# Optimization experiments

Hardware: AMD Instinct MI355X
Metric: run time of the kernel (lower is better)

The kernel has to match this reference:

```python
import jax, jax.numpy as jnp
import numpy as np

LEAK = 0.2
NUM_GRAPHS = 64


def _gat(h_in, src, dst, eh, W, att_src, att_dst, att_edge, lin_edge_W, bias, N):
    # PyG GATConv with edge_dim, concat=False (mean over heads)
    H, C = att_src.shape
    h = (h_in @ W).reshape(N, H, C)                      # [N,H,C]
    e = (eh @ lin_edge_W).reshape(-1, H, C)              # [Eaug,H,C]
    a_s = jnp.einsum('nhc,hc->nh', h, att_src)           # [N,H]
    a_d = jnp.einsum('nhc,hc->nh', h, att_dst)
    a_e = jnp.einsum('ehc,hc->eh', e, att_edge)          # [Eaug,H]
    score = jax.nn.leaky_relu(a_s[src] + a_d[dst] + a_e, LEAK)
    # scatter-softmax over incoming edges of each destination node
    m = jax.ops.segment_max(score, dst, num_segments=N)
    ex = jnp.exp(score - m[dst])
    den = jax.ops.segment_sum(ex, dst, num_segments=N)
    alpha = ex / den[dst]                                # [Eaug,H]
    out = jax.ops.segment_sum(alpha[:, :, None] * h[src], dst, num_segments=N)
    return out.mean(axis=1) + bias                       # concat=False -> head mean


def setup_inputs() -> dict:
    key = jax.random.key(0)
    ks = jax.random.split(key, 32)
    N, E, F, FE, HID, H, NT = 30000, 480000, 64, 16, 64, 4, 16
    Cin1 = F + HID
    s = 0.05
    d = {
        'x': jax.random.normal(ks[0], (N, F), jnp.float32),
        'edge_attr': jax.random.normal(ks[1], (E, FE), jnp.float32),
        'node_emb': jax.random.normal(ks[2], (NT, HID), jnp.float32) * s,
        'edge_W': jax.random.normal(ks[3], (FE, HID), jnp.float32) * s,
        'edge_b': jnp.zeros((HID,), jnp.float32),
        'W1': jax.random.normal(ks[4], (Cin1, H * HID), jnp.float32) * s,
        'as1': jax.random.normal(ks[5], (H, HID), jnp.float32) * s,
        'ad1': jax.random.normal(ks[6], (H, HID), jnp.float32) * s,
        'ae1': jax.random.normal(ks[7], (H, HID), jnp.float32) * s,
        'leW1': jax.random.normal(ks[8], (HID, H * HID), jnp.float32) * s,
        'b1': jnp.zeros((HID,), jnp.float32),
        'W2': jax.random.normal(ks[9], (HID, H * HID), jnp.float32) * s,
        'as2': jax.random.normal(ks[10], (H, HID), jnp.float32) * s,
        'ad2': jax.random.normal(ks[11], (H, HID), jnp.float32) * s,
        'ae2': jax.random.normal(ks[12], (H, HID), jnp.float32) * s,
        'leW2': jax.random.normal(ks[13], (HID, H * HID), jnp.float32) * s,
        'b2': jnp.zeros((HID,), jnp.float32),
        'sage_Wl': jax.random.normal(ks[14], (HID, HID), jnp.float32) * s,
        'sage_bl': jnp.zeros((HID,), jnp.float32),
        'sage_Wr': jax.random.normal(ks[15], (HID, HID), jnp.float32) * s,
        'lin1_W': jax.random.normal(ks[16], (HID, HID), jnp.float32) * s,
        'lin1_b': jnp.zeros((HID,), jnp.float32),
        'lin2_W': jax.random.normal(ks[17], (HID, HID), jnp.float32) * s,
        'lin2_b': jnp.zeros((HID,), jnp.float32),
        'tel_W': jax.random.normal(ks[18], (HID, 1), jnp.float32) * s,
        'tel_b': jnp.zeros((1,), jnp.float32),
        'comp_W': jax.random.normal(ks[19], (HID, 1), jnp.float32) * s,
        'comp_b': jnp.zeros((1,), jnp.float32),
        'pch_W': jax.random.normal(ks[20], (HID, 1), jnp.float32) * s,
        'pch_b': jnp.zeros((1,), jnp.float32),
        'edge_index': jax.random.randint(ks[21], (2, E), 0, N, jnp.int32),
        'batch': jnp.sort(jax.random.randint(ks[22], (N,), 0, NUM_GRAPHS, jnp.int32)),
        'node_type': jax.random.randint(ks[23], (N,), 0, NT, jnp.int32),
    }
    return d


def reference(x, edge_attr, node_emb, edge_W, edge_b,
              W1, as1, ad1, ae1, leW1, b1,
              W2, as2, ad2, ae2, leW2, b2,
              sage_Wl, sage_bl, sage_Wr,
              lin1_W, lin1_b, lin2_W, lin2_b,
              tel_W, tel_b, comp_W, comp_b, pch_W, pch_b,
              edge_index, batch, node_type):
    N = x.shape[0]
    src0, dst0 = edge_index[0], edge_index[1]

    h0 = jnp.concatenate([x, node_emb[node_type]], axis=-1)   # [N, F+HID]
    eh = edge_attr @ edge_W + edge_b                          # [E, HID]

    # GATConv default add_self_loops=True, fill_value='mean' on edge_attr
    loop = jnp.arange(N, dtype=src0.dtype)
    src = jnp.concatenate([src0, loop])
    dst = jnp.concatenate([dst0, loop])
    eh_aug = jnp.concatenate([eh, jnp.broadcast_to(eh.mean(axis=0), (N, eh.shape[1]))], axis=0)

    h1 = jax.nn.elu(_gat(h0, src, dst, eh_aug, W1, as1, ad1, ae1, leW1, b1, N))
    h2 = jax.nn.elu(_gat(h1, src, dst, eh_aug, W2, as2, ad2, ae2, leW2, b2, N))

    # SAGEConv: mean neighbor aggregation (src->dst) + root transform
    deg = jax.ops.segment_sum(jnp.ones_like(dst0, dtype=h2.dtype), dst0, num_segments=N)
    agg = jax.ops.segment_sum(h2[src0], dst0, num_segments=N) / jnp.clip(deg, 1.0)[:, None]
    h3 = jax.nn.elu(agg @ sage_Wl + sage_bl + h2 @ sage_Wr)

    # global mean pool per graph
    cnt = jax.ops.segment_sum(jnp.ones((N,), h3.dtype), batch, num_segments=NUM_GRAPHS)
    g = jax.ops.segment_sum(h3, batch, num_segments=NUM_GRAPHS) / jnp.clip(cnt, 1.0)[:, None]

    g = jax.nn.elu(g @ lin1_W + lin1_b)                       # dropout inactive (eval)
    g = g @ lin2_W + lin2_b
    return (g @ tel_W + tel_b, g @ comp_W + comp_b, g @ pch_W + pch_b)
```

## Files before the change

### kernel.cpp

```cpp
#include <hip/hip_runtime.h>
#include <math.h>

#define NN 30000
#define NE 480000
#define FEA 16
#define HID 64
#define NG 64
#define LEAKK 0.2f

#define S_MEANEA 0
#define S_KF1    16
#define S_C1     80
#define S_AEL1   84
#define S_KF2    88
#define S_C2     152
#define S_AEL2   156
#define S_MS1    160
#define S_MD1    672
#define S_MS2    1184
#define S_MD2    1440

__device__ __forceinline__ float eluf(float v) { return v > 0.f ? v : expm1f(v); }
__device__ __forceinline__ float leakyf(float v) { return v >= 0.f ? v : LEAKK * v; }
__device__ __forceinline__ void fma4(float4& a, float w, const float4& x) {
    a.x += w * x.x; a.y += w * x.y; a.z += w * x.z; a.w += w * x.w;
}
__device__ __forceinline__ unsigned bf16pack(float a, float b) {
    unsigned ua = __float_as_uint(a), ub = __float_as_uint(b);
    ua = (ua + 0x7FFFu + ((ua >> 16) & 1u)) >> 16;
    ub = (ub + 0x7FFFu + ((ub >> 16) & 1u)) >> 16;
    return ua | (ub << 16);
}
__device__ __forceinline__ float4 bf16x4(uint2 p) {
    float4 r;
    r.x = __uint_as_float(p.x << 16);
    r.y = __uint_as_float(p.x & 0xFFFF0000u);
    r.z = __uint_as_float(p.y << 16);
    r.w = __uint_as_float(p.y & 0xFFFF0000u);
    return r;
}

__global__ __launch_bounds__(256) void cm_prepw_kernel(
    const int* __restrict__ dst, const float* __restrict__ EA,
    int* __restrict__ cnt, int* __restrict__ rank, float* __restrict__ S,
    const float* __restrict__ W1, const float* __restrict__ W2,
    const float* __restrict__ Wl, const float* __restrict__ Wr,
    const float* __restrict__ emb,
    float* __restrict__ WC1, float* __restrict__ WC2, float* __restrict__ B128) {
    __shared__ float red[1024];
    int t = threadIdx.x;
    if (blockIdx.x < 176) {
        int i = blockIdx.x * 256 + t;
        if (i < 16384) {
            int hk = i >> 6, c = i & 63;
            int h = hk >> 6, k = hk & 63;
            WC1[i] = 0.25f * W1[k * 256 + h * 64 + c];
        } else if (i < 20480) {
            int j2 = i - 16384;
            int r2 = j2 >> 6, c = j2 & 63;
            int h = r2 >> 4, tau = r2 & 15;
            float v = 0.f;
            for (int j = 0; j < 64; j++)
                v += emb[tau * 64 + j] * W1[(64 + j) * 256 + h * 64 + c];
            WC1[i] = 0.25f * v;
        } else if (i < 36864) {
            int j = i - 20480;
            int hk = j >> 6, c = j & 63;
            int h = hk >> 6, k = hk & 63;
            WC2[j] = 0.25f * W2[k * 256 + h * 64 + c];
        } else if (i < 45056) {
            int j = i - 36864;
            int k = j >> 6, c = j & 63;
            B128[j] = (k < 64) ? Wl[k * 64 + c] : Wr[(k - 64) * 64 + c];
        }
        return;
    }
    int base = (blockIdx.x - 176) * 512;
#pragma unroll
    for (int i = 0; i < 2; i++) {
        int e = base + i * 256 + t;
        if (e < NE) rank[e] = atomicAdd(&cnt[dst[e]], 1);
    }
    int c4 = t & 3;
    int rbase = base + (t >> 2);
    float4 acc = {0, 0, 0, 0};
#pragma unroll
    for (int i = 0; i < 8; i++) {
        int r = rbase + i * 64;
        if (r < NE) {
            float4 v = *(const float4*)(EA + (size_t)r * FEA + c4 * 4);
            acc.x += v.x; acc.y += v.y; acc.z += v.z; acc.w += v.w;
        }
    }
    *(float4*)&red[t * 4] = acc;
    __syncthreads();
    if (t < 16) {
        int grp = t >> 2;
        int comp = t & 3;
        float sum = 0.f;
        for (int j = 0; j < 64; j++) sum += red[(grp + 4 * j) * 4 + comp];
        atomicAdd(&S[S_MEANEA + grp * 4 + comp], sum);
    }
}

__global__ void scan_blocks_kernel(const int* __restrict__ cnt, int* __restrict__ eoff,
                                   int* __restrict__ bsum) {
    __shared__ int wsum[16];
    int t = threadIdx.x;
    int i = blockIdx.x * 1024 + t;
    int v = (i < NN) ? cnt[i] : 0;
    int lane = t & 63;
    int incl = v;
#pragma unroll
    for (int ofs = 1; ofs < 64; ofs <<= 1) {
        int u = __shfl_up(incl, ofs, 64);
        if (lane >= ofs) incl += u;
    }
    int wid = t >> 6;
    if (lane == 63) wsum[wid] = incl;
    __syncthreads();
    if (t < 16) {
        int s = wsum[t];
#pragma unroll
        for (int ofs = 1; ofs < 16; ofs <<= 1) {
            int u = __shfl_up(s, ofs, 64);
            if (t >= ofs) s += u;
        }
        wsum[t] = s;
    }
    __syncthreads();
    int excl = incl - v + (wid > 0 ? wsum[wid - 1] : 0);
    if (i < NN) eoff[i] = excl;
    if (t == 1023) bsum[blockIdx.x] = excl + v;
}

__global__ void tops_goff_prep_kernel(
    const int* __restrict__ bsum, int* __restrict__ boff, int nb,
    const int* __restrict__ batch, int* __restrict__ goff,
    const float* __restrict__ W1, const float* __restrict__ as1, const float* __restrict__ ad1,
    const float* __restrict__ ae1, const float* __restrict__ leW1,
    const float* __restrict__ W2, const float* __restrict__ as2, const float* __restrict__ ad2,
    const float* __restrict__ ae2, const float* __restrict__ leW2,
    const float* __restrict__ edge_W, const float* __restrict__ edge_b,
    float* __restrict__ S) {
    __shared__ float M1[256], M2[256], meh[64];
    int t = threadIdx.x;
    if (blockIdx.x == 0) {
        if (t >= 64) return;
        int v = (t < nb) ? bsum[t] : 0;
        int incl = v;
#pragma unroll
        for (int ofs = 1; ofs < 64; ofs <<= 1) {
            int u = __shfl_up(incl, ofs, 64);
            if (t >= ofs) incl += u;
        }
        boff[t] = incl - v;
        return;
    }
    if (blockIdx.x == 1) {
        if (t > NG) return;
        int lo = 0, hi = NN;
        while (lo < hi) {
            int mid = (lo + hi) >> 1;
            if (batch[mid] < t) lo = mid + 1; else hi = mid;
        }
        goff[t] = lo;
        return;
    }
    if (t < 16) S[S_MEANEA + t] *= (1.0f / (float)NE);
    __syncthreads();
    {
        int k = t >> 2, h = t & 3;
        float m1 = 0.f, m2 = 0.f;
        for (int c = 0; c < 64; c++) {
            m1 += leW1[k * 256 + h * 64 + c] * ae1[h * 64 + c];
            m2 += leW2[k * 256 + h * 64 + c] * ae2[h * 64 + c];
        }
        M1[t] = m1; M2[t] = m2;
    }
    if (t < 64) {
        float v = edge_b[t];
        for (int f = 0; f < FEA; f++) v += S[S_MEANEA + f] * edge_W[f * 64 + t];
        meh[t] = v;
    }
    __syncthreads();
    if (t < 64) {
        int f = t >> 2, h = t & 3;
        float k1 = 0.f, k2 = 0.f;
        for (int k = 0; k < 64; k++) {
            k1 += edge_W[f * 64 + k] * M1[k * 4 + h];
            k2 += edge_W[f * 64 + k] * M2[k * 4 + h];
        }
        S[S_KF1 + t] = k1; S[S_KF2 + t] = k2;
    } else if (t < 68) {
        int h = t - 64;
        float c1 = 0.f, c2 = 0.f, a1 = 0.f, a2 = 0.f;
        for (int k = 0; k < 64; k++) {
            c1 += edge_b[k] * M1[k * 4 + h];
            c2 += edge_b[k] * M2[k * 4 + h];
            a1 += meh[k] * M1[k * 4 + h];
            a2 += meh[k] * M2[k * 4 + h];
        }
        S[S_C1 + h] = c1; S[S_C2 + h] = c2;
        S[S_AEL1 + h] = a1; S[S_AEL2 + h] = a2;
    }
    for (int i = t; i < 512; i += 256) {
        int k = i >> 2, h = i & 3;
        float s = 0.f, d = 0.f;
        for (int c = 0; c < 64; c++) {
            float w = W1[k * 256 + h * 64 + c];
            s += w * as1[h * 64 + c];
            d += w * ad1[h * 64 + c];
        }
        S[S_MS1 + i] = s; S[S_MD1 + i] = d;
    }
    for (int i = t; i < 256; i += 256) {
        int k = i >> 2, h = i & 3;
        float s = 0.f, d = 0.f;
        for (int c = 0; c < 64; c++) {
            float w = W2[k * 256 + h * 64 + c];
            s += w * as2[h * 64 + c];
            d += w * ad2[h * 64 + c];
        }
        S[S_MS2 + i] = s; S[S_MD2 + i] = d;
    }
}

__global__ __launch_bounds__(256) void scanadd_attn_kernel(
    const int* __restrict__ boff, int* __restrict__ eoff,
    const float* __restrict__ x, const float* __restrict__ node_emb,
    const int* __restrict__ node_type, const float* __restrict__ S,
    float* __restrict__ as_, float* __restrict__ ad_, unsigned* __restrict__ xb) {
    __shared__ float xt[64 * 132];
    __shared__ float ms[512], md[512];
    __shared__ int ntS[64];
    int t = threadIdx.x;
    if (blockIdx.x < 118) {
        int i = blockIdx.x * 256 + t;
        if (i < NN) eoff[i] += boff[i >> 10];
        if (i == 0) eoff[NN] = NE;
        return;
    }
    int n0 = (blockIdx.x - 118) * 64;
    if (t < 64) {
        int n = n0 + t;
        ntS[t] = (n < NN) ? node_type[n] : 0;
    }
    for (int i = t; i < 512; i += 256) { ms[i] = S[S_MS1 + i]; md[i] = S[S_MD1 + i]; }
    __syncthreads();
    for (int i = t; i < 1024; i += 256) {
        int r = i >> 4, c4 = (i & 15) * 4;
        int n = n0 + r;
        float4 f = {0, 0, 0, 0};
        if (n < NN) f = *(const float4*)(x + (size_t)n * 64 + c4);
        *(float4*)&xt[r * 132 + c4] = f;
    }
    for (int i = t; i < 1024; i += 256) {
        int r = i >> 4, c4 = (i & 15) * 4;
        int n = n0 + r;
        float4 f = {0, 0, 0, 0};
        if (n < NN) f = *(const float4*)(node_emb + (size_t)ntS[r] * 64 + c4);
        *(float4*)&xt[r * 132 + 64 + c4] = f;
    }
    __syncthreads();
    for (int i = t; i < 2048; i += 256) {
        int r = i >> 5, u = i & 31;
        int n = n0 + r;
        if (n < NN)
            xb[(size_t)n * 32 + u] = bf16pack(xt[r * 132 + 2 * u], xt[r * 132 + 2 * u + 1]);
    }
    int r = t >> 2, h = t & 3;
    float s = 0.f, d = 0.f;
#pragma unroll 8
    for (int k = 0; k < 128; k++) {
        float xv = xt[r * 132 + k];
        s += xv * ms[k * 4 + h];
        d += xv * md[k * 4 + h];
    }
    int n = n0 + r;
    if (n < NN) { as_[n * 4 + h] = s; ad_[n * 4 + h] = d; }
}

__global__ void scatter_score_kernel(const int* __restrict__ src, const int* __restrict__ dst,
                                     const float* __restrict__ EA, const float* __restrict__ S,
                                     const float* __restrict__ as_, const float* __restrict__ ad_,
                                     const int* __restrict__ node_type,
                                     const int* __restrict__ eoff, const int* __restrict__ rank,
                                     int2* __restrict__ se_sorted,
                                     float* __restrict__ sc1, float* __restrict__ ae2s) {
    int e = blockIdx.x * 256 + threadIdx.x;
    if (e >= NE) return;
    int s = src[e], d = dst[e];
    float a1[4], a2[4];
#pragma unroll
    for (int h = 0; h < 4; h++) { a1[h] = S[S_C1 + h]; a2[h] = S[S_C2 + h]; }
    const float4* EA4 = (const float4*)(EA + (size_t)e * FEA);
#pragma unroll
    for (int q = 0; q < 4; q++) {
        float4 v = EA4[q];
        float vv[4] = {v.x, v.y, v.z, v.w};
#pragma unroll
        for (int j = 0; j < 4; j++) {
            int f = q * 4 + j;
#pragma unroll
            for (int h = 0; h < 4; h++) {
                a1[h] += vv[j] * S[S_KF1 + f * 4 + h];
                a2[h] += vv[j] * S[S_KF2 + f * 4 + h];
            }
        }
    }
    ((float4*)ae2s)[e] = make_float4(a2[0], a2[1], a2[2], a2[3]);
    float4 asv = ((const float4*)as_)[s];
    float4 adv = ((const float4*)ad_)[d];
    float4 r;
    r.x = expf(leakyf(asv.x + adv.x + a1[0]));
    r.y = expf(leakyf(asv.y + adv.y + a1[1]));
    r.z = expf(leakyf(asv.z + adv.z + a1[2]));
    r.w = expf(leakyf(asv.w + adv.w + a1[3]));
    ((float4*)sc1)[e] = r;
    int ty = node_type[s];
    se_sorted[eoff[d] + rank[e]] = make_int2(s, e | (ty << 24));
}

__global__ void score2_kernel(const int* __restrict__ src, const int* __restrict__ dst,
                              const float* __restrict__ ae2s,
                              const float* __restrict__ as_, const float* __restrict__ ad_,
                              float* __restrict__ sc2) {
    int e = blockIdx.x * 256 + threadIdx.x;
    if (e >= NE) return;
    int s = src[e], d = dst[e];
    float4 ae = ((const float4*)ae2s)[e];
    float4 asv = ((const float4*)as_)[s];
    float4 adv = ((const float4*)ad_)[d];
    float4 r;
    r.x = expf(leakyf(asv.x + adv.x + ae.x));
    r.y = expf(leakyf(asv.y + adv.y + ae.y));
    r.z = expf(leakyf(asv.z + adv.z + ae.z));
    r.w = expf(leakyf(asv.w + adv.w + ae.w));
    ((float4*)sc2)[e] = r;
}

__global__ __launch_bounds__(256) void agg_gat1_kernel(
    const int* __restrict__ eoff, const int2* __restrict__ se_sorted,
    const float* __restrict__ sc1, const unsigned* __restrict__ xb,
    const int* __restrict__ node_type,
    const float* __restrict__ as_, const float* __restrict__ ad_,
    const float* __restrict__ Sael, float* __restrict__ agg) {
    int n = blockIdx.x * 4 + (threadIdx.x >> 6);
    if (n >= NN) return;
    int lane = threadIdx.x & 63;
    int sub = lane >> 4, ch = lane & 15;
    const uint2* Xb = (const uint2*)xb;
    const float4* W4 = (const float4*)sc1;
    float4 asn = ((const float4*)as_)[n];
    float4 adn = ((const float4*)ad_)[n];
    float4 a0 = {0, 0, 0, 0}, a1 = a0, a2 = a0, a3 = a0, dn = a0, tw = a0;
    int b = eoff[n], e_end = eoff[n + 1];
    int nE = e_end - b;
    int i = sub;
    for (; i + 4 < nE; i += 8) {
        int2 se0 = se_sorted[b + i], se1 = se_sorted[b + i + 4];
        int e0 = se0.y & 0xFFFFFF, t0 = se0.y >> 24;
        int e1 = se1.y & 0xFFFFFF, t1 = se1.y >> 24;
        float4 w0 = W4[e0], w1 = W4[e1];
        float4 x0 = bf16x4(Xb[(size_t)se0.x * 16 + ch]);
        float4 x1 = bf16x4(Xb[(size_t)se1.x * 16 + ch]);
        fma4(a0, w0.x, x0); fma4(a1, w0.y, x0); fma4(a2, w0.z, x0); fma4(a3, w0.w, x0);
        fma4(a0, w1.x, x1); fma4(a1, w1.y, x1); fma4(a2, w1.z, x1); fma4(a3, w1.w, x1);
        dn.x += w0.x + w1.x; dn.y += w0.y + w1.y;
        dn.z += w0.z + w1.z; dn.w += w0.w + w1.w;
        if (ch == t0) { tw.x += w0.x; tw.y += w0.y; tw.z += w0.z; tw.w += w0.w; }
        if (ch == t1) { tw.x += w1.x; tw.y += w1.y; tw.z += w1.z; tw.w += w1.w; }
    }
    for (; i < nE; i += 4) {
        int2 se0 = se_sorted[b + i];
        int e0 = se0.y & 0xFFFFFF, t0 = se0.y >> 24;
        float4 w0 = W4[e0];
        float4 x0 = bf16x4(Xb[(size_t)se0.x * 16 + ch]);
        fma4(a0, w0.x, x0); fma4(a1, w0.y, x0); fma4(a2, w0.z, x0); fma4(a3, w0.w, x0);
        dn.x += w0.x; dn.y += w0.y; dn.z += w0.z; dn.w += w0.w;
        if (ch == t0) { tw.x += w0.x; tw.y += w0.y; tw.z += w0.z; tw.w += w0.w; }
    }
    if (sub == 0) {
        float e0 = expf(leakyf(asn.x + adn.x + Sael[0]));
        float e1 = expf(leakyf(asn.y + adn.y + Sael[1]));
        float e2 = expf(leakyf(asn.z + adn.z + Sael[2]));
        float e3 = expf(leakyf(asn.w + adn.w + Sael[3]));
        float4 xs = bf16x4(Xb[(size_t)n * 16 + ch]);
        fma4(a0, e0, xs); fma4(a1, e1, xs); fma4(a2, e2, xs); fma4(a3, e3, xs);
        dn.x += e0; dn.y += e1; dn.z += e2; dn.w += e3;
        int tn = node_type[n];
        if (ch == tn) { tw.x += e0; tw.y += e1; tw.z += e2; tw.w += e3; }
    }
#pragma unroll
    for (int mask = 16; mask < 64; mask <<= 1) {
        a0.x += __shfl_xor(a0.x, mask, 64); a0.y += __shfl_xor(a0.y, mask, 64);
        a0.z += __shfl_xor(a0.z, mask, 64); a0.w += __shfl_xor(a0.w, mask, 64);
        a1.x += __shfl_xor(a1.x, mask, 64); a1.y += __shfl_xor(a1.y, mask, 64);
        a1.z += __shfl_xor(a1.z, mask, 64); a1.w += __shfl_xor(a1.w, mask, 64);
        a2.x += __shfl_xor(a2.x, mask, 64); a2.y += __shfl_xor(a2.y, mask, 64);
        a2.z += __shfl_xor(a2.z, mask, 64); a2.w += __shfl_xor(a2.w, mask, 64);
        a3.x += __shfl_xor(a3.x, mask, 64); a3.y += __shfl_xor(a3.y, mask, 64);
        a3.z += __shfl_xor(a3.z, mask, 64); a3.w += __shfl_xor(a3.w, mask, 64);
        dn.x += __shfl_xor(dn.x, mask, 64); dn.y += __shfl_xor(dn.y, mask, 64);
        dn.z += __shfl_xor(dn.z, mask, 64); dn.w += __shfl_xor(dn.w, mask, 64);
        tw.x += __shfl_xor(tw.x, mask, 64); tw.y += __shfl_xor(tw.y, mask, 64);
        tw.z += __shfl_xor(tw.z, mask, 64); tw.w += __shfl_xor(tw.w, mask, 64);
    }
    if (sub == 0) {
        float i0 = 1.f / dn.x, i1 = 1.f / dn.y, i2 = 1.f / dn.z, i3 = 1.f / dn.w;
        float* A = agg + (size_t)n * 320;
        float4* A4 = (float4*)A;
        A4[ch]      = make_float4(a0.x * i0, a0.y * i0, a0.z * i0, a0.w * i0);
        A4[16 + ch] = make_float4(a1.x * i1, a1.y * i1, a1.z * i1, a1.w * i1);
        A4[32 + ch] = make_float4(a2.x * i2, a2.y * i2, a2.z * i2, a2.w * i2);
        A4[48 + ch] = make_float4(a3.x * i3, a3.y * i3, a3.z * i3, a3.w * i3);
        A[256 + ch]      = tw.x * i0;
        A[256 + 16 + ch] = tw.y * i1;
        A[256 + 32 + ch] = tw.z * i2;
        A[256 + 48 + ch] = tw.w * i3;
    }
}

__global__ __launch_bounds__(256) void agg_gat2_kernel(
    const int* __restrict__ eoff, const int2* __restrict__ se_sorted,
    const float* __restrict__ sc2, const unsigned* __restrict__ h1b,
    const float* __restrict__ as_, const float* __restrict__ ad_,
    const float* __restrict__ Sael, float* __restrict__ agg) {
    int n = blockIdx.x * 4 + (threadIdx.x >> 6);
    if (n >= NN) return;
    int lane = threadIdx.x & 63;
    int sub = lane >> 4, ch = lane & 15;
    const uint2* Xb = (const uint2*)h1b;
    const float4* W4 = (const float4*)sc2;
    float4 asn = ((const float4*)as_)[n];
    float4 adn = ((const float4*)ad_)[n];
    float4 a0 = {0, 0, 0, 0}, a1 = a0, a2 = a0, a3 = a0, dn = a0;
    int b = eoff[n], e = eoff[n + 1];
    int nE = e - b;
    int i = sub;
    for (; i + 4 < nE; i += 8) {
        int2 se0 = se_sorted[b + i], se1 = se_sorted[b + i + 4];
        float4 w0 = W4[se0.y & 0xFFFFFF], w1 = W4[se1.y & 0xFFFFFF];
        float4 x0 = bf16x4(Xb[(size_t)se0.x * 16 + ch]);
        float4 x1 = bf16x4(Xb[(size_t)se1.x * 16 + ch]);
        fma4(a0, w0.x, x0); fma4(a1, w0.y, x0); fma4(a2, w0.z, x0); fma4(a3, w0.w, x0);
        fma4(a0, w1.x, x1); fma4(a1, w1.y, x1); fma4(a2, w1.z, x1); fma4(a3, w1.w, x1);
        dn.x += w0.x + w1.x; dn.y += w0.y + w1.y;
        dn.z += w0.z + w1.z; dn.w += w0.w + w1.w;
    }
    for (; i < nE; i += 4) {
        int2 se0 = se_sorted[b + i];
        float4 w0 = W4[se0.y & 0xFFFFFF];
        float4 x0 = bf16x4(Xb[(size_t)se0.x * 16 + ch]);
        fma4(a0, w0.x, x0); fma4(a1, w0.y, x0); fma4(a2, w0.z, x0); fma4(a3, w0.w, x0);
        dn.x += w0.x; dn.y += w0.y; dn.z += w0.z; dn.w += w0.w;
    }
    if (sub == 0) {
        float e0 = expf(leakyf(asn.x + adn.x + Sael[0]));
        float e1 = expf(leakyf(asn.y + adn.y + Sael[1]));
        float e2 = expf(leakyf(asn.z + adn.z + Sael[2]));
        float e3 = expf(leakyf(asn.w + adn.w + Sael[3]));
        float4 xs = bf16x4(Xb[(size_t)n * 16 + ch]);
        fma4(a0, e0, xs); fma4(a1, e1, xs); fma4(a2, e2, xs); fma4(a3, e3, xs);
        dn.x += e0; dn.y += e1; dn.z += e2; dn.w += e3;
    }
#pragma unroll
    for (int mask = 16; mask < 64; mask <<= 1) {
        a0.x += __shfl_xor(a0.x, mask, 64); a0.y += __shfl_xor(a0.y, mask, 64);
        a0.z += __shfl_xor(a0.z, mask, 64); a0.w += __shfl_xor(a0.w, mask, 64);
        a1.x += __shfl_xor(a1.x, mask, 64); a1.y += __shfl_xor(a1.y, mask, 64);
        a1.z += __shfl_xor(a1.z, mask, 64); a1.w += __shfl_xor(a1.w, mask, 64);
        a2.x += __shfl_xor(a2.x, mask, 64); a2.y += __shfl_xor(a2.y, mask, 64);
        a2.z += __shfl_xor(a2.z, mask, 64); a2.w += __shfl_xor(a2.w, mask, 64);
        a3.x += __shfl_xor(a3.x, mask, 64); a3.y += __shfl_xor(a3.y, mask, 64);
        a3.z += __shfl_xor(a3.z, mask, 64); a3.w += __shfl_xor(a3.w, mask, 64);
        dn.x += __shfl_xor(dn.x, mask, 64); dn.y += __shfl_xor(dn.y, mask, 64);
        dn.z += __shfl_xor(dn.z, mask, 64); dn.w += __shfl_xor(dn.w, mask, 64);
    }
    if (sub == 0) {
        float i0 = 1.f / dn.x, i1 = 1.f / dn.y, i2 = 1.f / dn.z, i3 = 1.f / dn.w;
        float4* agg4 = (float4*)(agg + (size_t)n * 256);
        agg4[ch]      = make_float4(a0.x * i0, a0.y * i0, a0.z * i0, a0.w * i0);
        agg4[16 + ch] = make_float4(a1.x * i1, a1.y * i1, a1.z * i1, a1.w * i1);
        agg4[32 + ch] = make_float4(a2.x * i2, a2.y * i2, a2.z * i2, a2.w * i2);
        agg4[48 + ch] = make_float4(a3.x * i3, a3.y * i3, a3.z * i3, a3.w * i3);
    }
}

template <int K, bool DOATT>
__global__ __launch_bounds__(256) void gemm64_kernel(
    const float* __restrict__ A, const float* __restrict__ B,
    const float* __restrict__ bias, float* __restrict__ out,
    unsigned* __restrict__ out16,
    const float* __restrict__ ms_g, const float* __restrict__ md_g,
    float* __restrict__ as_, float* __restrict__ ad_) {
    __shared__ float As[2][32 * 68];
    __shared__ float Bs[2][32 * 68];
    __shared__ float msS[256], mdS[256];
    int t = threadIdx.x;
    int tx = t & 15, ty = t >> 4;
    int m_base = blockIdx.x * 64;
    if (DOATT) { msS[t] = ms_g[t]; mdS[t] = md_g[t]; }
    int arow0 = t >> 3, akq0 = (t & 7) * 4;
    int arow1 = (t + 256) >> 3, akq1 = ((t + 256) & 7) * 4;
    int bkr = t >> 4, bnc = (t & 15) * 4;
    int am0 = m_base + arow0, am1 = m_base + arow1;
    float4 fa0, fa1, fb0, fb1;
    fa0 = (am0 < NN) ? *(const float4*)(A + (size_t)am0 * K + akq0) : make_float4(0, 0, 0, 0);
    fa1 = (am1 < NN) ? *(const float4*)(A + (size_t)am1 * K + akq1) : make_float4(0, 0, 0, 0);
    fb0 = *(const float4*)(B + (size_t)bkr * 64 + bnc);
    fb1 = *(const float4*)(B + (size_t)(bkr + 16) * 64 + bnc);
    As[0][(akq0 + 0) * 68 + arow0] = fa0.x;
    As[0][(akq0 + 1) * 68 + arow0] = fa0.y;
    As[0][(akq0 + 2) * 68 + arow0] = fa0.z;
    As[0][(akq0 + 3) * 68 + arow0] = fa0.w;
    As[0][(akq1 + 0) * 68 + arow1] = fa1.x;
    As[0][(akq1 + 1) * 68 + arow1] = fa1.y;
    As[0][(akq1 + 2) * 68 + arow1] = fa1.z;
    As[0][(akq1 + 3) * 68 + arow1] = fa1.w;
    *(float4*)&Bs[0][bkr * 68 + bnc] = fb0;
    *(float4*)&Bs[0][(bkr + 16) * 68 + bnc] = fb1;
    __syncthreads();
    float acc[4][4] = {};
    int cur = 0;
    for (int k0 = 0;; k0 += 32) {
        bool more = (k0 + 32 < K);
        if (more) {
            int kn = k0 + 32;
            fa0 = (am0 < NN) ? *(const float4*)(A + (size_t)am0 * K + kn + akq0)
                             : make_float4(0, 0, 0, 0);
            fa1 = (am1 < NN) ? *(const float4*)(A + (size_t)am1 * K + kn + akq1)
                             : make_float4(0, 0, 0, 0);
            fb0 = *(const float4*)(B + (size_t)(kn + bkr) * 64 + bnc);
            fb1 = *(const float4*)(B + (size_t)(kn + bkr + 16) * 64 + bnc);
        }
#pragma unroll
        for (int k = 0; k < 32; k++) {
            float4 av = *(const float4*)&As[cur][k * 68 + ty * 4];
            float4 bv = *(const float4*)&Bs[cur][k * 68 + tx * 4];
            float a[4] = {av.x, av.y, av.z, av.w};
            float b[4] = {bv.x, bv.y, bv.z, bv.w};
#pragma unroll
            for (int i = 0; i < 4; i++)
#pragma unroll
                for (int j = 0; j < 4; j++) acc[i][j] += a[i] * b[j];
        }
        if (!more) break;
        int nxt = cur ^ 1;
        As[nxt][(akq0 + 0) * 68 + arow0] = fa0.x;
        As[nxt][(akq0 + 1) * 68 + arow0] = fa0.y;
        As[nxt][(akq0 + 2) * 68 + arow0] = fa0.z;
        As[nxt][(akq0 + 3) * 68 + arow0] = fa0.w;
        As[nxt][(akq1 + 0) * 68 + arow1] = fa1.x;
        As[nxt][(akq1 + 1) * 68 + arow1] = fa1.y;
        As[nxt][(akq1 + 2) * 68 + arow1] = fa1.z;
        As[nxt][(akq1 + 3) * 68 + arow1] = fa1.w;
        *(float4*)&Bs[nxt][bkr * 68 + bnc] = fb0;
        *(float4*)&Bs[nxt][(bkr + 16) * 68 + bnc] = fb1;
        __syncthreads();
        cur = nxt;
    }
    float4 bvv = ((const float4*)bias)[tx];
    float o[4][4];
#pragma unroll
    for (int i = 0; i < 4; i++) {
        o[i][0] = eluf(acc[i][0] + bvv.x);
        o[i][1] = eluf(acc[i][1] + bvv.y);
        o[i][2] = eluf(acc[i][2] + bvv.z);
        o[i][3] = eluf(acc[i][3] + bvv.w);
        int m = m_base + ty * 4 + i;
        if (m < NN) {
            *(float4*)(out + (size_t)m * 64 + tx * 4) =
                make_float4(o[i][0], o[i][1], o[i][2], o[i][3]);
            if (out16) {
                out16[(size_t)m * 32 + tx * 2]     = bf16pack(o[i][0], o[i][1]);
                out16[(size_t)m * 32 + tx * 2 + 1] = bf16pack(o[i][2], o[i][3]);
            }
        }
    }
    if (DOATT) {
        float ps[4][4] = {}, pd[4][4] = {};
#pragma unroll
        for (int i = 0; i < 4; i++)
#pragma unroll
            for (int j = 0; j < 4; j++) {
                float v = o[i][j];
                int kk = (tx * 4 + j) * 4;
#pragma unroll
                for (int h = 0; h < 4; h++) {
                    ps[i][h] += v * msS[kk + h];
                    pd[i][h] += v * mdS[kk + h];
                }
            }
#pragma unroll
        for (int mk = 1; mk < 16; mk <<= 1) {
#pragma unroll
            for (int i = 0; i < 4; i++)
#pragma unroll
                for (int h = 0; h < 4; h++) {
                    ps[i][h] += __shfl_xor(ps[i][h], mk, 64);
                    pd[i][h] += __shfl_xor(pd[i][h], mk, 64);
                }
        }
        if (tx == 0) {
#pragma unroll
            for (int i = 0; i < 4; i++) {
                int m = m_base + ty * 4 + i;
                if (m < NN) {
                    *(float4*)(as_ + (size_t)m * 4) =
                        make_float4(ps[i][0], ps[i][1], ps[i][2], ps[i][3]);
                    *(float4*)(ad_ + (size_t)m * 4) =
                        make_float4(pd[i][0], pd[i][1], pd[i][2], pd[i][3]);
                }
            }
        }
    }
}

__global__ __launch_bounds__(256) void sage_agg3_kernel(
    const float* __restrict__ h2, const unsigned* __restrict__ h2b,
    const int* __restrict__ eoff, const int2* __restrict__ se_sorted,
    float* __restrict__ AB) {
    int n = blockIdx.x * 16 + (threadIdx.x >> 4);
    if (n >= NN) return;
    int l = threadIdx.x & 15;
    const uint2* Hb = (const uint2*)h2b;
    const float4* h24 = (const float4*)h2;
    float4* AB4 = (float4*)AB;
    float ax = 0.f, ay = 0.f, az = 0.f, aw = 0.f;
    int b = eoff[n], e_end = eoff[n + 1];
    int idx = b;
    int stop = b + ((e_end - b) & ~7);
    if (idx < stop) {
        int sreg[8];
#pragma unroll
        for (int u = 0; u < 8; u++) sreg[u] = se_sorted[idx + u].x;
        idx += 8;
        while (true) {
            int sn[8];
            bool more = idx < stop;
            if (more) {
#pragma unroll
                for (int u = 0; u < 8; u++) sn[u] = se_sorted[idx + u].x;
            }
#pragma unroll
            for (int u = 0; u < 8; u++) {
                float4 v = bf16x4(Hb[(size_t)sreg[u] * 16 + l]);
                ax += v.x; ay += v.y; az += v.z; aw += v.w;
            }
            if (!more) break;
#pragma unroll
            for (int u = 0; u < 8; u++) sreg[u] = sn[u];
            idx += 8;
        }
    }
    for (; idx < e_end; idx++) {
        float4 v0 = bf16x4(Hb[(size_t)se_sorted[idx].x * 16 + l]);
        ax += v0.x; ay += v0.y; az += v0.z; aw += v0.w;
    }
    float dg = (float)(e_end - b);
    if (dg < 1.f) dg = 1.f;
    float inv = 1.f / dg;
    AB4[(size_t)n * 32 + l] = make_float4(ax * inv, ay * inv, az * inv, aw * inv);
    AB4[(size_t)n * 32 + 16 + l] = h24[(size_t)n * 16 + l];
}

__global__ __launch_bounds__(256) void pool_mlp_kernel(
    const float* __restrict__ h3, const int* __restrict__ goff,
    const float* __restrict__ lin1W, const float* __restrict__ lin1b,
    const float* __restrict__ lin2W, const float* __restrict__ lin2b,
    const float* __restrict__ telW, const float* __restrict__ telb,
    const float* __restrict__ compW, const float* __restrict__ compb,
    const float* __restrict__ pchW, const float* __restrict__ pchb,
    float* __restrict__ out) {
    __shared__ float red[256];
    __shared__ float g[64], G1[64], G2[64];
    int gi = blockIdx.x, t = threadIdx.x;
    int c = t & 63, li = t >> 6;
    int b = goff[gi], e = goff[gi + 1];
    float sum = 0.f;
    for (int r = b + li; r < e; r += 4) sum += h3[(size_t)r * HID + c];
    red[t] = sum;
    __syncthreads();
    if (t < 64) {
        float v = red[t] + red[t + 64] + red[t + 128] + red[t + 192];
        float cntf = (float)(e - b);
        if (cntf < 1.f) cntf = 1.f;
        g[t] = v / cntf;
    }
    __syncthreads();
    {
        float part = 0.f;
#pragma unroll
        for (int k = li * 16; k < li * 16 + 16; k++) part += g[k] * lin1W[k * 64 + c];
        red[t] = part;
        __syncthreads();
        if (t < 64)
            G1[c] = eluf(red[c] + red[c + 64] + red[c + 128] + red[c + 192] + lin1b[c]);
        __syncthreads();
    }
    {
        float part = 0.f;
#pragma unroll
        for (int k = li * 16; k < li * 16 + 16; k++) part += G1[k] * lin2W[k * 64 + c];
        red[t] = part;
        __syncthreads();
        if (t < 64)
            G2[c] = red[c] + red[c + 64] + red[c + 128] + red[c + 192] + lin2b[c];
        __syncthreads();
    }
    if (t < 192) {
        int h = t >> 6, k = t & 63;
        const float* W = (h == 0) ? telW : ((h == 1) ? compW : pchW);
        red[t] = G2[k] * W[k];
    }
    __syncthreads();
    if (t < 3) {
        float acc = 0.f;
        for (int k = 0; k < 64; k++) acc += red[t * 64 + k];
        float bb = (t == 0) ? telb[0] : ((t == 1) ? compb[0] : pchb[0]);
        out[t * 64 + gi] = acc + bb;
    }
}

extern "C" void kernel_launch(void* const* d_in, const int* in_sizes, int n_in,
                              void* d_out, int out_size, void* d_ws, size_t ws_size,
                              hipStream_t stream) {
    const float* x        = (const float*)d_in[0];
    const float* EA       = (const float*)d_in[1];
    const float* node_emb = (const float*)d_in[2];
    const float* edge_W   = (const float*)d_in[3];
    const float* edge_b   = (const float*)d_in[4];
    const float* W1       = (const float*)d_in[5];
    const float* as1      = (const float*)d_in[6];
    const float* ad1      = (const float*)d_in[7];
    const float* ae1      = (const float*)d_in[8];
    const float* leW1     = (const float*)d_in[9];
    const float* b1       = (const float*)d_in[10];
    const float* W2       = (const float*)d_in[11];
    const float* as2      = (const float*)d_in[12];
    const float* ad2      = (const float*)d_in[13];
    const float* ae2      = (const float*)d_in[14];
    const float* leW2     = (const float*)d_in[15];
    const float* b2       = (const float*)d_in[16];
    const float* sage_Wl  = (const float*)d_in[17];
    const float* sage_bl  = (const float*)d_in[18];
    const float* sage_Wr  = (const float*)d_in[19];
    const float* lin1_W   = (const float*)d_in[20];
    const float* lin1_b   = (const float*)d_in[21];
    const float* lin2_W   = (const float*)d_in[22];
    const float* lin2_b   = (const float*)d_in[23];
    const float* tel_W    = (const float*)d_in[24];
    const float* tel_b    = (const float*)d_in[25];
    const float* comp_W   = (const float*)d_in[26];
    const float* comp_b   = (const float*)d_in[27];
    const float* pch_W    = (const float*)d_in[28];
    const float* pch_b    = (const float*)d_in[29];
    const int* edge_index = (const int*)d_in[30];
    const int* batch      = (const int*)d_in[31];
    const int* node_type  = (const int*)d_in[32];
    float* outp = (float*)d_out;

    const int* srcp = edge_index;
    const int* dstp = edge_index + NE;

    float* wf = (float*)d_ws;
    constexpr size_t OFF_H3    = 0;
    constexpr size_t OFF_AGG   = OFF_H3 + (size_t)NN * 64;
    constexpr size_t OFF_H1    = OFF_AGG + (size_t)NN * 512;
    constexpr size_t OFF_H2    = OFF_H1 + (size_t)NN * 64;
    constexpr size_t OFF_SC    = OFF_H2 + (size_t)NN * 64;
    constexpr size_t OFF_AE2   = OFF_SC + (size_t)NE * 4;
    constexpr size_t OFF_AS    = OFF_AE2 + (size_t)NE * 4;
    constexpr size_t OFF_AD    = OFF_AS + (size_t)NN * 4;
    constexpr size_t OFF_SMALL = OFF_AD + (size_t)NN * 4;
    constexpr size_t OFF_WC1   = OFF_SMALL + 4096;
    constexpr size_t OFF_WC2   = OFF_WC1 + 20480;
    constexpr size_t OFF_B128  = OFF_WC2 + 16384;
    constexpr size_t OFF_XB    = OFF_B128 + 8192;
    constexpr size_t OFF_H1B   = OFF_XB + (size_t)NN * 32;
    constexpr size_t OFF_H2B   = OFF_H1B + (size_t)NN * 32;
    constexpr size_t F_TOTAL   = OFF_H2B + (size_t)NN * 32;

    int* wi         = (int*)(wf + F_TOTAL);
    int* cnt        = wi;
    int* rank       = wi + NN;
    int* eoff       = rank + NE;
    int2* se_sorted = (int2*)(eoff + (NN + 2));
    int* goff       = (int*)(se_sorted + NE);
    int* bsum       = goff + (NG + 1);
    int* boff       = bsum + 64;

    float* h3    = wf + OFF_H3;
    float* aggb  = wf + OFF_AGG;
    float* h1    = wf + OFF_H1;
    float* h2    = wf + OFF_H2;
    float* sc    = wf + OFF_SC;
    float* ae2s  = wf + OFF_AE2;
    float* as_   = wf + OFF_AS;
    float* ad_   = wf + OFF_AD;
    float* S     = wf + OFF_SMALL;
    float* WC1   = wf + OFF_WC1;
    float* WC2   = wf + OFF_WC2;
    float* B128  = wf + OFF_B128;
    unsigned* xb  = (unsigned*)(wf + OFF_XB);
    unsigned* h1b = (unsigned*)(wf + OFF_H1B);
    unsigned* h2b = (unsigned*)(wf + OFF_H2B);
    float* AB    = wf + OFF_AGG;

    hipMemsetAsync(S + S_MEANEA, 0, 16 * sizeof(float), stream);
    hipMemsetAsync(cnt, 0, NN * sizeof(int), stream);

    cm_prepw_kernel<<<176 + (NE + 511) / 512, 256, 0, stream>>>(
        dstp, EA, cnt, rank, S, W1, W2, sage_Wl, sage_Wr, node_emb, WC1, WC2, B128);
    {
        int nb = (NN + 1023) / 1024;
        scan_blocks_kernel<<<nb, 1024, 0, stream>>>(cnt, eoff, bsum);
        tops_goff_prep_kernel<<<3, 256, 0, stream>>>(
            bsum, boff, nb, batch, goff,
            W1, as1, ad1, ae1, leW1, W2, as2, ad2, ae2, leW2, edge_W, edge_b, S);
        scanadd_attn_kernel<<<118 + (NN + 63) / 64, 256, 0, stream>>>(
            boff, eoff, x, node_emb, node_type, S, as_, ad_, xb);
    }
    scatter_score_kernel<<<(NE + 255) / 256, 256, 0, stream>>>(
        srcp, dstp, EA, S, as_, ad_, node_type, eoff, rank, se_sorted, sc, ae2s);

    agg_gat1_kernel<<<(NN + 3) / 4, 256, 0, stream>>>(
        eoff, se_sorted, sc, xb, node_type, as_, ad_, S + S_AEL1, aggb);
    gemm64_kernel<320, true><<<(NN + 63) / 64, 256, 0, stream>>>(
        aggb, WC1, b1, h1, h1b, S + S_MS2, S + S_MD2, as_, ad_);

    score2_kernel<<<(NE + 255) / 256, 256, 0, stream>>>(srcp, dstp, ae2s, as_, ad_, sc);
    agg_gat2_kernel<<<(NN + 3) / 4, 256, 0, stream>>>(
        eoff, se_sorted, sc, h1b, as_, ad_, S + S_AEL2, aggb);
    gemm64_kernel<256, false><<<(NN + 63) / 64, 256, 0, stream>>>(
        aggb, WC2, b2, h2, h2b, nullptr, nullptr, nullptr, nullptr);

    sage_agg3_kernel<<<(NN + 15) / 16, 256, 0, stream>>>(h2, h2b, eoff, se_sorted, AB);
    gemm64_kernel<128, false><<<(NN + 63) / 64, 256, 0, stream>>>(
        AB, B128, sage_bl, h3, nullptr, nullptr, nullptr, nullptr, nullptr);

    pool_mlp_kernel<<<NG, 256, 0, stream>>>(h3, goff, lin1_W, lin1_b, lin2_W, lin2_b,
                                            tel_W, tel_b, comp_W, comp_b, pch_W, pch_b, outp);
}
```

Baseline: 404.9 us.

## Fuse edge-attention into prep, store scores sorted, compute GAT2 scores inline, bf16 aggregates

Edge attention projections for both layers are now computed in the prep kernel while it already streams edge_attr, which removes the second edge pass in scatter_score. Layer-1 scores are written in dst-sorted order, so agg_gat1 reads them contiguously instead of gathering them by edge id. The separate score2 kernel is dropped and agg_gat2 recomputes its scores inline from as/ad/ae2. All intermediate aggregate buffers feeding the GEMMs are stored as bf16 and the unused fp32 h1/h2 outputs are skipped, cutting memory traffic at some precision cost. The WC1 type-embedding row ordering is also changed to tau-major to match the new layout.

```diff
diff --git a/kernel.cpp b/kernel.cpp
--- a/kernel.cpp
+++ b/kernel.cpp
@@ -9,11 +9,7 @@
 #define LEAKK 0.2f
 
 #define S_MEANEA 0
-#define S_KF1    16
-#define S_C1     80
 #define S_AEL1   84
-#define S_KF2    88
-#define S_C2     152
 #define S_AEL2   156
 #define S_MS1    160
 #define S_MD1    672
@@ -30,6 +26,9 @@
     ua = (ua + 0x7FFFu + ((ua >> 16) & 1u)) >> 16;
     ub = (ub + 0x7FFFu + ((ub >> 16) & 1u)) >> 16;
     return ua | (ub << 16);
+}
+__device__ __forceinline__ uint2 bfpack4(float a, float b, float c, float d) {
+    return make_uint2(bf16pack(a, b), bf16pack(c, d));
 }
 __device__ __forceinline__ float4 bf16x4(uint2 p) {
     float4 r;
@@ -39,6 +38,14 @@
     r.w = __uint_as_float(p.y & 0xFFFF0000u);
     return r;
 }
+__device__ __forceinline__ float4 escore4(float4 a, float4 b, float4 c) {
+    float4 r;
+    r.x = expf(leakyf(a.x + b.x + c.x));
+    r.y = expf(leakyf(a.y + b.y + c.y));
+    r.z = expf(leakyf(a.z + b.z + c.z));
+    r.w = expf(leakyf(a.w + b.w + c.w));
+    return r;
+}
 
 __global__ __launch_bounds__(256) void cm_prepw_kernel(
     const int* __restrict__ dst, const float* __restrict__ EA,
@@ -46,8 +53,11 @@
     const float* __restrict__ W1, const float* __restrict__ W2,
     const float* __restrict__ Wl, const float* __restrict__ Wr,
     const float* __restrict__ emb,
-    float* __restrict__ WC1, float* __restrict__ WC2, float* __restrict__ B128) {
-    __shared__ float red[1024];
+    const float* __restrict__ leW1, const float* __restrict__ aew1,
+    const float* __restrict__ leW2, const float* __restrict__ aew2,
+    const float* __restrict__ edge_W, const float* __restrict__ edge_b,
+    float* __restrict__ WC1, float* __restrict__ WC2, float* __restrict__ B128,
+    float* __restrict__ ae1s, float* __restrict__ ae2s) {
     int t = threadIdx.x;
     if (blockIdx.x < 176) {
         int i = blockIdx.x * 256 + t;
@@ -58,7 +68,7 @@
         } else if (i < 20480) {
             int j2 = i - 16384;
             int r2 = j2 >> 6, c = j2 & 63;
-            int h = r2 >> 4, tau = r2 & 15;
+            int tau = r2 >> 2, h = r2 & 3;
             float v = 0.f;
             for (int j = 0; j < 64; j++)
                 v += emb[tau * 64 + j] * W1[(64 + j) * 256 + h * 64 + c];
@@ -75,32 +85,82 @@
         }
         return;
     }
+    __shared__ float M1s[256], M2s[256];
+    __shared__ float KF1[64], KF2[64], C1s[4], C2s[4];
+    __shared__ float wred[4][16];
+    {
+        int k = t >> 2, h = t & 3;
+        float m1 = 0.f, m2 = 0.f;
+        for (int c = 0; c < 64; c++) {
+            m1 += leW1[k * 256 + h * 64 + c] * aew1[h * 64 + c];
+            m2 += leW2[k * 256 + h * 64 + c] * aew2[h * 64 + c];
+        }
+        M1s[t] = m1; M2s[t] = m2;
+    }
+    __syncthreads();
+    if (t < 64) {
+        int f = t >> 2, h = t & 3;
+        float k1 = 0.f, k2 = 0.f;
+        for (int k = 0; k < 64; k++) {
+            k1 += edge_W[f * 64 + k] * M1s[k * 4 + h];
+            k2 += edge_W[f * 64 + k] * M2s[k * 4 + h];
+        }
+        KF1[t] = k1; KF2[t] = k2;
+    } else if (t < 68) {
+        int h = t - 64;
+        float c1 = 0.f, c2 = 0.f;
+        for (int k = 0; k < 64; k++) {
+            c1 += edge_b[k] * M1s[k * 4 + h];
+            c2 += edge_b[k] * M2s[k * 4 + h];
+        }
+        C1s[h] = c1; C2s[h] = c2;
+    }
+    __syncthreads();
     int base = (blockIdx.x - 176) * 512;
+    float facc[16];
+#pragma unroll
+    for (int f = 0; f < 16; f++) facc[f] = 0.f;
 #pragma unroll
     for (int i = 0; i < 2; i++) {
         int e = base + i * 256 + t;
-        if (e < NE) rank[e] = atomicAdd(&cnt[dst[e]], 1);
-    }
-    int c4 = t & 3;
-    int rbase = base + (t >> 2);
-    float4 acc = {0, 0, 0, 0};
-#pragma unroll
-    for (int i = 0; i < 8; i++) {
-        int r = rbase + i * 64;
-        if (r < NE) {
-            float4 v = *(const float4*)(EA + (size_t)r * FEA + c4 * 4);
-            acc.x += v.x; acc.y += v.y; acc.z += v.z; acc.w += v.w;
-        }
-    }
-    *(float4*)&red[t * 4] = acc;
-    __syncthreads();
-    if (t < 16) {
-        int grp = t >> 2;
-        int comp = t & 3;
-        float sum = 0.f;
-        for (int j = 0; j < 64; j++) sum += red[(grp + 4 * j) * 4 + comp];
-        atomicAdd(&S[S_MEANEA + grp * 4 + comp], sum);
-    }
+        if (e < NE) {
+            rank[e] = atomicAdd(&cnt[dst[e]], 1);
+            float a1[4], a2[4];
+#pragma unroll
+            for (int h = 0; h < 4; h++) { a1[h] = C1s[h]; a2[h] = C2s[h]; }
+            const float4* EA4 = (const float4*)(EA + (size_t)e * FEA);
+#pragma unroll
+            for (int q = 0; q < 4; q++) {
+                float4 v = EA4[q];
+                float vv[4] = {v.x, v.y, v.z, v.w};
+#pragma unroll
+                for (int j = 0; j < 4; j++) {
+                    int f = q * 4 + j;
+                    facc[f] += vv[j];
+#pragma unroll
+                    for (int h = 0; h < 4; h++) {
+                        a1[h] += vv[j] * KF1[f * 4 + h];
+                        a2[h] += vv[j] * KF2[f * 4 + h];
+                    }
+                }
+            }
+            ((float4*)ae1s)[e] = make_float4(a1[0], a1[1], a1[2], a1[3]);
+            ((float4*)ae2s)[e] = make_float4(a2[0], a2[1], a2[2], a2[3]);
+        }
+    }
+#pragma unroll
+    for (int mask = 1; mask < 64; mask <<= 1) {
+#pragma unroll
+        for (int f = 0; f < 16; f++) facc[f] += __shfl_xor(facc[f], mask, 64);
+    }
+    int wid = t >> 6, lane = t & 63;
+    if (lane == 0) {
+#pragma unroll
+        for (int f = 0; f < 16; f++) wred[wid][f] = facc[f];
+    }
+    __syncthreads();
+    if (t < 16)
+        atomicAdd(&S[S_MEANEA + t], wred[0][t] + wred[1][t] + wred[2][t] + wred[3][t]);
 }
 
 __global__ void scan_blocks_kernel(const int* __restrict__ cnt, int* __restrict__ eoff,
@@ -184,25 +244,14 @@
         meh[t] = v;
     }
     __syncthreads();
-    if (t < 64) {
-        int f = t >> 2, h = t & 3;
-        float k1 = 0.f, k2 = 0.f;
+    if (t >= 64 && t < 68) {
+        int h = t - 64;
+        float a1v = 0.f, a2v = 0.f;
         for (int k = 0; k < 64; k++) {
-            k1 += edge_W[f * 64 + k] * M1[k * 4 + h];
-            k2 += edge_W[f * 64 + k] * M2[k * 4 + h];
-        }
-        S[S_KF1 + t] = k1; S[S_KF2 + t] = k2;
-    } else if (t < 68) {
-        int h = t - 64;
-        float c1 = 0.f, c2 = 0.f, a1 = 0.f, a2 = 0.f;
-        for (int k = 0; k < 64; k++) {
-            c1 += edge_b[k] * M1[k * 4 + h];
-            c2 += edge_b[k] * M2[k * 4 + h];
-            a1 += meh[k] * M1[k * 4 + h];
-            a2 += meh[k] * M2[k * 4 + h];
-        }
-        S[S_C1 + h] = c1; S[S_C2 + h] = c2;
-        S[S_AEL1 + h] = a1; S[S_AEL2 + h] = a2;
+            a1v += meh[k] * M1[k * 4 + h];
+            a2v += meh[k] * M2[k * 4 + h];
+        }
+        S[S_AEL1 + h] = a1v; S[S_AEL2 + h] = a2v;
     }
     for (int i = t; i < 512; i += 256) {
         int k = i >> 2, h = i & 3;
@@ -281,77 +330,38 @@
     if (n < NN) { as_[n * 4 + h] = s; ad_[n * 4 + h] = d; }
 }
 
-__global__ void scatter_score_kernel(const int* __restrict__ src, const int* __restrict__ dst,
-                                     const float* __restrict__ EA, const float* __restrict__ S,
-                                     const float* __restrict__ as_, const float* __restrict__ ad_,
-                                     const int* __restrict__ node_type,
-                                     const int* __restrict__ eoff, const int* __restrict__ rank,
-                                     int2* __restrict__ se_sorted,
-                                     float* __restrict__ sc1, float* __restrict__ ae2s) {
+__global__ __launch_bounds__(256) void scatter_score_kernel(
+    const int* __restrict__ src, const int* __restrict__ dst,
+    const float* __restrict__ ae1s,
+    const float* __restrict__ as_, const float* __restrict__ ad_,
+    const int* __restrict__ node_type,
+    const int* __restrict__ eoff, const int* __restrict__ rank,
+    int2* __restrict__ se_sorted, float* __restrict__ scs) {
     int e = blockIdx.x * 256 + threadIdx.x;
     if (e >= NE) return;
     int s = src[e], d = dst[e];
-    float a1[4], a2[4];
-#pragma unroll
-    for (int h = 0; h < 4; h++) { a1[h] = S[S_C1 + h]; a2[h] = S[S_C2 + h]; }
-    const float4* EA4 = (const float4*)(EA + (size_t)e * FEA);
-#pragma unroll
-    for (int q = 0; q < 4; q++) {
-        float4 v = EA4[q];
-        float vv[4] = {v.x, v.y, v.z, v.w};
-#pragma unroll
-        for (int j = 0; j < 4; j++) {
-            int f = q * 4 + j;
-#pragma unroll
-            for (int h = 0; h < 4; h++) {
-                a1[h] += vv[j] * S[S_KF1 + f * 4 + h];
-                a2[h] += vv[j] * S[S_KF2 + f * 4 + h];
-            }
-        }
-    }
-    ((float4*)ae2s)[e] = make_float4(a2[0], a2[1], a2[2], a2[3]);
+    float4 a1 = ((const float4*)ae1s)[e];
     float4 asv = ((const float4*)as_)[s];
     float4 adv = ((const float4*)ad_)[d];
-    float4 r;
-    r.x = expf(leakyf(asv.x + adv.x + a1[0]));
-    r.y = expf(leakyf(asv.y + adv.y + a1[1]));
-    r.z = expf(leakyf(asv.z + adv.z + a1[2]));
-    r.w = expf(leakyf(asv.w + adv.w + a1[3]));
-    ((float4*)sc1)[e] = r;
+    float4 r = escore4(asv, adv, a1);
+    int pos = eoff[d] + rank[e];
+    ((float4*)scs)[pos] = r;
     int ty = node_type[s];
-    se_sorted[eoff[d] + rank[e]] = make_int2(s, e | (ty << 24));
-}
-
-__global__ void score2_kernel(const int* __restrict__ src, const int* __restrict__ dst,
-                              const float* __restrict__ ae2s,
-                              const float* __restrict__ as_, const float* __restrict__ ad_,
-                              float* __restrict__ sc2) {
-    int e = blockIdx.x * 256 + threadIdx.x;
-    if (e >= NE) return;
-    int s = src[e], d = dst[e];
-    float4 ae = ((const float4*)ae2s)[e];
-    float4 asv = ((const float4*)as_)[s];
-    float4 adv = ((const float4*)ad_)[d];
-    float4 r;
-    r.x = expf(leakyf(asv.x + adv.x + ae.x));
-    r.y = expf(leakyf(asv.y + adv.y + ae.y));
-    r.z = expf(leakyf(asv.z + adv.z + ae.z));
-    r.w = expf(leakyf(asv.w + adv.w + ae.w));
-    ((float4*)sc2)[e] = r;
+    se_sorted[pos] = make_int2(s, e | (ty << 24));
 }
 
 __global__ __launch_bounds__(256) void agg_gat1_kernel(
     const int* __restrict__ eoff, const int2* __restrict__ se_sorted,
-    const float* __restrict__ sc1, const unsigned* __restrict__ xb,
+    const float* __restrict__ scs, const unsigned* __restrict__ xb,
     const int* __restrict__ node_type,
     const float* __restrict__ as_, const float* __restrict__ ad_,
-    const float* __restrict__ Sael, float* __restrict__ agg) {
+    const float* __restrict__ Sael, uint2* __restrict__ aggb) {
     int n = blockIdx.x * 4 + (threadIdx.x >> 6);
     if (n >= NN) return;
     int lane = threadIdx.x & 63;
     int sub = lane >> 4, ch = lane & 15;
     const uint2* Xb = (const uint2*)xb;
-    const float4* W4 = (const float4*)sc1;
+    const float4* W4 = (const float4*)scs;
     float4 asn = ((const float4*)as_)[n];
     float4 adn = ((const float4*)ad_)[n];
     float4 a0 = {0, 0, 0, 0}, a1 = a0, a2 = a0, a3 = a0, dn = a0, tw = a0;
@@ -360,9 +370,8 @@
     int i = sub;
     for (; i + 4 < nE; i += 8) {
         int2 se0 = se_sorted[b + i], se1 = se_sorted[b + i + 4];
-        int e0 = se0.y & 0xFFFFFF, t0 = se0.y >> 24;
-        int e1 = se1.y & 0xFFFFFF, t1 = se1.y >> 24;
-        float4 w0 = W4[e0], w1 = W4[e1];
+        int t0 = se0.y >> 24, t1 = se1.y >> 24;
+        float4 w0 = W4[b + i], w1 = W4[b + i + 4];
         float4 x0 = bf16x4(Xb[(size_t)se0.x * 16 + ch]);
         float4 x1 = bf16x4(Xb[(size_t)se1.x * 16 + ch]);
         fma4(a0, w0.x, x0); fma4(a1, w0.y, x0); fma4(a2, w0.z, x0); fma4(a3, w0.w, x0);
@@ -374,8 +383,8 @@
     }
     for (; i < nE; i += 4) {
         int2 se0 = se_sorted[b + i];
-        int e0 = se0.y & 0xFFFFFF, t0 = se0.y >> 24;
-        float4 w0 = W4[e0];
+        int t0 = se0.y >> 24;
+        float4 w0 = W4[b + i];
         float4 x0 = bf16x4(Xb[(size_t)se0.x * 16 + ch]);
         fma4(a0, w0.x, x0); fma4(a1, w0.y, x0); fma4(a2, w0.z, x0); fma4(a3, w0.w, x0);
         dn.x += w0.x; dn.y += w0.y; dn.z += w0.z; dn.w += w0.w;
@@ -409,31 +418,28 @@
     }
     if (sub == 0) {
         float i0 = 1.f / dn.x, i1 = 1.f / dn.y, i2 = 1.f / dn.z, i3 = 1.f / dn.w;
-        float* A = agg + (size_t)n * 320;
-        float4* A4 = (float4*)A;
-        A4[ch]      = make_float4(a0.x * i0, a0.y * i0, a0.z * i0, a0.w * i0);
-        A4[16 + ch] = make_float4(a1.x * i1, a1.y * i1, a1.z * i1, a1.w * i1);
-        A4[32 + ch] = make_float4(a2.x * i2, a2.y * i2, a2.z * i2, a2.w * i2);
-        A4[48 + ch] = make_float4(a3.x * i3, a3.y * i3, a3.z * i3, a3.w * i3);
-        A[256 + ch]      = tw.x * i0;
-        A[256 + 16 + ch] = tw.y * i1;
-        A[256 + 32 + ch] = tw.z * i2;
-        A[256 + 48 + ch] = tw.w * i3;
+        uint2* A2 = aggb + (size_t)n * 80;
+        A2[ch]      = bfpack4(a0.x * i0, a0.y * i0, a0.z * i0, a0.w * i0);
+        A2[16 + ch] = bfpack4(a1.x * i1, a1.y * i1, a1.z * i1, a1.w * i1);
+        A2[32 + ch] = bfpack4(a2.x * i2, a2.y * i2, a2.z * i2, a2.w * i2);
+        A2[48 + ch] = bfpack4(a3.x * i3, a3.y * i3, a3.z * i3, a3.w * i3);
+        A2[64 + ch] = bfpack4(tw.x * i0, tw.y * i1, tw.z * i2, tw.w * i3);
     }
 }
 
 __global__ __launch_bounds__(256) void agg_gat2_kernel(
     const int* __restrict__ eoff, const int2* __restrict__ se_sorted,
-    const float* __restrict__ sc2, const unsigned* __restrict__ h1b,
+    const float* __restrict__ ae2s, const unsigned* __restrict__ h1b,
     const float* __restrict__ as_, const float* __restrict__ ad_,
-    const float* __restrict__ Sael, float* __restrict__ agg) {
+    const float* __restrict__ Sael, uint2* __restrict__ aggb) {
     int n = blockIdx.x * 4 + (threadIdx.x >> 6);
     if (n >= NN) return;
     int lane = threadIdx.x & 63;
     int sub = lane >> 4, ch = lane & 15;
     const uint2* Xb = (const uint2*)h1b;
-    const float4* W4 = (const float4*)sc2;
-    float4 asn = ((const float4*)as_)[n];
+    const float4* AE4 = (const float4*)ae2s;
+    const float4* AS4 = (const float4*)as_;
+    float4 asn = AS4[n];
     float4 adn = ((const float4*)ad_)[n];
     float4 a0 = {0, 0, 0, 0}, a1 = a0, a2 = a0, a3 = a0, dn = a0;
     int b = eoff[n], e = eoff[n + 1];
@@ -441,9 +447,13 @@
     int i = sub;
     for (; i + 4 < nE; i += 8) {
         int2 se0 = se_sorted[b + i], se1 = se_sorted[b + i + 4];
-        float4 w0 = W4[se0.y & 0xFFFFFF], w1 = W4[se1.y & 0xFFFFFF];
+        int e0 = se0.y & 0xFFFFFF, e1 = se1.y & 0xFFFFFF;
+        float4 q0 = AE4[e0], q1 = AE4[e1];
+        float4 s0 = AS4[se0.x], s1 = AS4[se1.x];
         float4 x0 = bf16x4(Xb[(size_t)se0.x * 16 + ch]);
         float4 x1 = bf16x4(Xb[(size_t)se1.x * 16 + ch]);
+        float4 w0 = escore4(s0, adn, q0);
+        float4 w1 = escore4(s1, adn, q1);
         fma4(a0, w0.x, x0); fma4(a1, w0.y, x0); fma4(a2, w0.z, x0); fma4(a3, w0.w, x0);
         fma4(a0, w1.x, x1); fma4(a1, w1.y, x1); fma4(a2, w1.z, x1); fma4(a3, w1.w, x1);
         dn.x += w0.x + w1.x; dn.y += w0.y + w1.y;
@@ -451,7 +461,8 @@
     }
     for (; i < nE; i += 4) {
         int2 se0 = se_sorted[b + i];
-        float4 w0 = W4[se0.y & 0xFFFFFF];
+        int e0 = se0.y & 0xFFFFFF;
+        float4 w0 = escore4(AS4[se0.x], adn, AE4[e0]);
         float4 x0 = bf16x4(Xb[(size_t)se0.x * 16 + ch]);
         fma4(a0, w0.x, x0); fma4(a1, w0.y, x0); fma4(a2, w0.z, x0); fma4(a3, w0.w, x0);
         dn.x += w0.x; dn.y += w0.y; dn.z += w0.z; dn.w += w0.w;
@@ -480,17 +491,17 @@
     }
     if (sub == 0) {
         float i0 = 1.f / dn.x, i1 = 1.f / dn.y, i2 = 1.f / dn.z, i3 = 1.f / dn.w;
-        float4* agg4 = (float4*)(agg + (size_t)n * 256);
-        agg4[ch]      = make_float4(a0.x * i0, a0.y * i0, a0.z * i0, a0.w * i0);
-        agg4[16 + ch] = make_float4(a1.x * i1, a1.y * i1, a1.z * i1, a1.w * i1);
-        agg4[32 + ch] = make_float4(a2.x * i2, a2.y * i2, a2.z * i2, a2.w * i2);
-        agg4[48 + ch] = make_float4(a3.x * i3, a3.y * i3, a3.z * i3, a3.w * i3);
+        uint2* A2 = aggb + (size_t)n * 64;
+        A2[ch]      = bfpack4(a0.x * i0, a0.y * i0, a0.z * i0, a0.w * i0);
+        A2[16 + ch] = bfpack4(a1.x * i1, a1.y * i1, a1.z * i1, a1.w * i1);
+        A2[32 + ch] = bfpack4(a2.x * i2, a2.y * i2, a2.z * i2, a2.w * i2);
+        A2[48 + ch] = bfpack4(a3.x * i3, a3.y * i3, a3.z * i3, a3.w * i3);
     }
 }
 
 template <int K, bool DOATT>
 __global__ __launch_bounds__(256) void gemm64_kernel(
-    const float* __restrict__ A, const float* __restrict__ B,
+    const unsigned* __restrict__ A, const float* __restrict__ B,
     const float* __restrict__ bias, float* __restrict__ out,
     unsigned* __restrict__ out16,
     const float* __restrict__ ms_g, const float* __restrict__ md_g,
@@ -502,23 +513,28 @@
     int tx = t & 15, ty = t >> 4;
     int m_base = blockIdx.x * 64;
     if (DOATT) { msS[t] = ms_g[t]; mdS[t] = md_g[t]; }
-    int arow0 = t >> 3, akq0 = (t & 7) * 4;
-    int arow1 = (t + 256) >> 3, akq1 = ((t + 256) & 7) * 4;
+    int arow = t >> 2, ak8 = (t & 3) * 8;
+    int am = m_base + arow;
     int bkr = t >> 4, bnc = (t & 15) * 4;
-    int am0 = m_base + arow0, am1 = m_base + arow1;
-    float4 fa0, fa1, fb0, fb1;
-    fa0 = (am0 < NN) ? *(const float4*)(A + (size_t)am0 * K + akq0) : make_float4(0, 0, 0, 0);
-    fa1 = (am1 < NN) ? *(const float4*)(A + (size_t)am1 * K + akq1) : make_float4(0, 0, 0, 0);
+    const uint4* A4 = (const uint4*)A;
+    const int arstride = K / 8;
+    uint4 ua;
+    float4 fb0, fb1;
+    ua = (am < NN) ? A4[(size_t)am * arstride + (ak8 >> 3)] : make_uint4(0, 0, 0, 0);
     fb0 = *(const float4*)(B + (size_t)bkr * 64 + bnc);
     fb1 = *(const float4*)(B + (size_t)(bkr + 16) * 64 + bnc);
-    As[0][(akq0 + 0) * 68 + arow0] = fa0.x;
-    As[0][(akq0 + 1) * 68 + arow0] = fa0.y;
-    As[0][(akq0 + 2) * 68 + arow0] = fa0.z;
-    As[0][(akq0 + 3) * 68 + arow0] = fa0.w;
-    As[0][(akq1 + 0) * 68 + arow1] = fa1.x;
-    As[0][(akq1 + 1) * 68 + arow1] = fa1.y;
-    As[0][(akq1 + 2) * 68 + arow1] = fa1.z;
-    As[0][(akq1 + 3) * 68 + arow1] = fa1.w;
+    {
+        float4 lo = bf16x4(make_uint2(ua.x, ua.y));
+        float4 hi = bf16x4(make_uint2(ua.z, ua.w));
+        As[0][(ak8 + 0) * 68 + arow] = lo.x;
+        As[0][(ak8 + 1) * 68 + arow] = lo.y;
+        As[0][(ak8 + 2) * 68 + arow] = lo.z;
+        As[0][(ak8 + 3) * 68 + arow] = lo.w;
+        As[0][(ak8 + 4) * 68 + arow] = hi.x;
+        As[0][(ak8 + 5) * 68 + arow] = hi.y;
+        As[0][(ak8 + 6) * 68 + arow] = hi.z;
+        As[0][(ak8 + 7) * 68 + arow] = hi.w;
+    }
     *(float4*)&Bs[0][bkr * 68 + bnc] = fb0;
     *(float4*)&Bs[0][(bkr + 16) * 68 + bnc] = fb1;
     __syncthreads();
@@ -528,10 +544,8 @@
         bool more = (k0 + 32 < K);
         if (more) {
             int kn = k0 + 32;
-            fa0 = (am0 < NN) ? *(const float4*)(A + (size_t)am0 * K + kn + akq0)
-                             : make_float4(0, 0, 0, 0);
-            fa1 = (am1 < NN) ? *(const float4*)(A + (size_t)am1 * K + kn + akq1)
-                             : make_float4(0, 0, 0, 0);
+            ua = (am < NN) ? A4[(size_t)am * arstride + ((kn + ak8) >> 3)]
+                           : make_uint4(0, 0, 0, 0);
             fb0 = *(const float4*)(B + (size_t)(kn + bkr) * 64 + bnc);
             fb1 = *(const float4*)(B + (size_t)(kn + bkr + 16) * 64 + bnc);
         }
@@ -548,14 +562,18 @@
         }
         if (!more) break;
         int nxt = cur ^ 1;
-        As[nxt][(akq0 + 0) * 68 + arow0] = fa0.x;
-        As[nxt][(akq0 + 1) * 68 + arow0] = fa0.y;
-        As[nxt][(akq0 + 2) * 68 + arow0] = fa0.z;
-        As[nxt][(akq0 + 3) * 68 + arow0] = fa0.w;
-        As[nxt][(akq1 + 0) * 68 + arow1] = fa1.x;
-        As[nxt][(akq1 + 1) * 68 + arow1] = fa1.y;
-        As[nxt][(akq1 + 2) * 68 + arow1] = fa1.z;
-        As[nxt][(akq1 + 3) * 68 + arow1] = fa1.w;
+        {
+            float4 lo = bf16x4(make_uint2(ua.x, ua.y));
+            float4 hi = bf16x4(make_uint2(ua.z, ua.w));
+            As[nxt][(ak8 + 0) * 68 + arow] = lo.x;
+            As[nxt][(ak8 + 1) * 68 + arow] = lo.y;
+            As[nxt][(ak8 + 2) * 68 + arow] = lo.z;
+            As[nxt][(ak8 + 3) * 68 + arow] = lo.w;
+            As[nxt][(ak8 + 4) * 68 + arow] = hi.x;
+            As[nxt][(ak8 + 5) * 68 + arow] = hi.y;
+            As[nxt][(ak8 + 6) * 68 + arow] = hi.z;
+            As[nxt][(ak8 + 7) * 68 + arow] = hi.w;
+        }
         *(float4*)&Bs[nxt][bkr * 68 + bnc] = fb0;
         *(float4*)&Bs[nxt][(bkr + 16) * 68 + bnc] = fb1;
         __syncthreads();
@@ -571,8 +589,9 @@
         o[i][3] = eluf(acc[i][3] + bvv.w);
         int m = m_base + ty * 4 + i;
         if (m < NN) {
-            *(float4*)(out + (size_t)m * 64 + tx * 4) =
-                make_float4(o[i][0], o[i][1], o[i][2], o[i][3]);
+            if (out)
+                *(float4*)(out + (size_t)m * 64 + tx * 4) =
+                    make_float4(o[i][0], o[i][1], o[i][2], o[i][3]);
             if (out16) {
                 out16[(size_t)m * 32 + tx * 2]     = bf16pack(o[i][0], o[i][1]);
                 out16[(size_t)m * 32 + tx * 2 + 1] = bf16pack(o[i][2], o[i][3]);
@@ -619,15 +638,13 @@
 }
 
 __global__ __launch_bounds__(256) void sage_agg3_kernel(
-    const float* __restrict__ h2, const unsigned* __restrict__ h2b,
+    const unsigned* __restrict__ h2b,
     const int* __restrict__ eoff, const int2* __restrict__ se_sorted,
-    float* __restrict__ AB) {
+    uint2* __restrict__ AB) {
     int n = blockIdx.x * 16 + (threadIdx.x >> 4);
     if (n >= NN) return;
     int l = threadIdx.x & 15;
     const uint2* Hb = (const uint2*)h2b;
-    const float4* h24 = (const float4*)h2;
-    float4* AB4 = (float4*)AB;
     float ax = 0.f, ay = 0.f, az = 0.f, aw = 0.f;
     int b = eoff[n], e_end = eoff[n + 1];
     int idx = b;
@@ -662,8 +679,8 @@
     float dg = (float)(e_end - b);
     if (dg < 1.f) dg = 1.f;
     float inv = 1.f / dg;
-    AB4[(size_t)n * 32 + l] = make_float4(ax * inv, ay * inv, az * inv, aw * inv);
-    AB4[(size_t)n * 32 + 16 + l] = h24[(size_t)n * 16 + l];
+    AB[(size_t)n * 32 + l] = bfpack4(ax * inv, ay * inv, az * inv, aw * inv);
+    AB[(size_t)n * 32 + 16 + l] = Hb[(size_t)n * 16 + l];
 }
 
 __global__ __launch_bounds__(256) void pool_mlp_kernel(
@@ -768,8 +785,8 @@
     float* wf = (float*)d_ws;
     constexpr size_t OFF_H3    = 0;
     constexpr size_t OFF_AGG   = OFF_H3 + (size_t)NN * 64;
-    constexpr size_t OFF_H1    = OFF_AGG + (size_t)NN * 512;
-    constexpr size_t OFF_H2    = OFF_H1 + (size_t)NN * 64;
+    constexpr size_t OFF_AE1   = OFF_AGG + (size_t)NN * 512;
+    constexpr size_t OFF_H2    = OFF_AE1 + (size_t)NE * 4;
     constexpr size_t OFF_SC    = OFF_H2 + (size_t)NN * 64;
     constexpr size_t OFF_AE2   = OFF_SC + (size_t)NE * 4;
     constexpr size_t OFF_AS    = OFF_AE2 + (size_t)NE * 4;
@@ -794,8 +811,7 @@
 
     float* h3    = wf + OFF_H3;
     float* aggb  = wf + OFF_AGG;
-    float* h1    = wf + OFF_H1;
-    float* h2    = wf + OFF_H2;
+    float* ae1s  = wf + OFF_AE1;
     float* sc    = wf + OFF_SC;
     float* ae2s  = wf + OFF_AE2;
     float* as_   = wf + OFF_AS;
@@ -807,13 +823,13 @@
     unsigned* xb  = (unsigned*)(wf + OFF_XB);
     unsigned* h1b = (unsigned*)(wf + OFF_H1B);
     unsigned* h2b = (unsigned*)(wf + OFF_H2B);
-    float* AB    = wf + OFF_AGG;
 
     hipMemsetAsync(S + S_MEANEA, 0, 16 * sizeof(float), stream);
     hipMemsetAsync(cnt, 0, NN * sizeof(int), stream);
 
     cm_prepw_kernel<<<176 + (NE + 511) / 512, 256, 0, stream>>>(
-        dstp, EA, cnt, rank, S, W1, W2, sage_Wl, sage_Wr, node_emb, WC1, WC2, B128);
+        dstp, EA, cnt, rank, S, W1, W2, sage_Wl, sage_Wr, node_emb,
+        leW1, ae1, leW2, ae2, edge_W, edge_b, WC1, WC2, B128, ae1s, ae2s);
     {
         int nb = (NN + 1023) / 1024;
         scan_blocks_kernel<<<nb, 1024, 0, stream>>>(cnt, eoff, bsum);
@@ -824,22 +840,21 @@
             boff, eoff, x, node_emb, node_type, S, as_, ad_, xb);
     }
     scatter_score_kernel<<<(NE + 255) / 256, 256, 0, stream>>>(
-        srcp, dstp, EA, S, as_, ad_, node_type, eoff, rank, se_sorted, sc, ae2s);
+        srcp, dstp, ae1s, as_, ad_, node_type, eoff, rank, se_sorted, sc);
 
     agg_gat1_kernel<<<(NN + 3) / 4, 256, 0, stream>>>(
-        eoff, se_sorted, sc, xb, node_type, as_, ad_, S + S_AEL1, aggb);
+        eoff, se_sorted, sc, xb, node_type, as_, ad_, S + S_AEL1, (uint2*)aggb);
     gemm64_kernel<320, true><<<(NN + 63) / 64, 256, 0, stream>>>(
-        aggb, WC1, b1, h1, h1b, S + S_MS2, S + S_MD2, as_, ad_);
-
-    score2_kernel<<<(NE + 255) / 256, 256, 0, stream>>>(srcp, dstp, ae2s, as_, ad_, sc);
+        (const unsigned*)aggb, WC1, b1, nullptr, h1b, S + S_MS2, S + S_MD2, as_, ad_);
+
     agg_gat2_kernel<<<(NN + 3) / 4, 256, 0, stream>>>(
-        eoff, se_sorted, sc, h1b, as_, ad_, S + S_AEL2, aggb);
+        eoff, se_sorted, ae2s, h1b, as_, ad_, S + S_AEL2, (uint2*)aggb);
     gemm64_kernel<256, false><<<(NN + 63) / 64, 256, 0, stream>>>(
-        aggb, WC2, b2, h2, h2b, nullptr, nullptr, nullptr, nullptr);
-
-    sage_agg3_kernel<<<(NN + 15) / 16, 256, 0, stream>>>(h2, h2b, eoff, se_sorted, AB);
+        (const unsigned*)aggb, WC2, b2, nullptr, h2b, nullptr, nullptr, nullptr, nullptr);
+
+    sage_agg3_kernel<<<(NN + 15) / 16, 256, 0, stream>>>(h2b, eoff, se_sorted, (uint2*)aggb);
     gemm64_kernel<128, false><<<(NN + 63) / 64, 256, 0, stream>>>(
-        AB, B128, sage_bl, h3, nullptr, nullptr, nullptr, nullptr, nullptr);
+        (const unsigned*)aggb, B128, sage_bl, h3, nullptr, nullptr, nullptr, nullptr, nullptr);
 
     pool_mlp_kernel<<<NG, 256, 0, stream>>>(h3, goff, lin1_W, lin1_b, lin2_W, lin2_b,
                                             tel_W, tel_b, comp_W, comp_b, pch_W, pch_b, outp);
```

Result: no change. 407.4 us (+0.6%).
